# Kernel tuning notes

Measured on AMD Instinct MI355X. Metric: run time of the kernel, lower is better.

The kernel has to match this reference:

```python
import jax, jax.numpy as jnp
import numpy as np


def _safe_div(w, n):
    # tf.math.divide_no_nan: returns 0 where denominator is 0
    n = n[:, None]
    return jnp.where(n > 0, w / jnp.where(n > 0, n, 1.0), 0.0)


def setup_inputs() -> dict:
    key = jax.random.key(0)
    x = jax.random.normal(key, (16, 32768, 256), dtype=jnp.float32)
    return {"x": x}


def reference(x):
    # x: [n_models, n_samples, dim]
    n_models = x.shape[0]
    xt = jnp.transpose(x, (1, 0, 2))  # [ns, nm, dim]
    v0 = xt[:, 0, :]
    basis_list = [_safe_div(v0, jnp.linalg.norm(v0, axis=1))]  # each [ns, dim]
    for i in range(1, n_models):
        B = jnp.stack(basis_list, axis=1)              # [ns, i, dim]
        v = xt[:, i, :]                                # [ns, dim]
        coef = jnp.einsum('nd,nid->ni', v, B)          # projections onto basis
        w = v - jnp.einsum('ni,nid->nd', coef, B)      # classical Gram-Schmidt step
        basis_list.append(_safe_div(w, jnp.linalg.norm(w, axis=1)))
    return jnp.stack(basis_list, axis=0)               # [n_models, ns, dim]
```

## Files before the change

### kernel.cpp

```cpp
#include <hip/hip_runtime.h>
#include <hip/hip_bf16.h>


constexpr int NM   = 16;
constexpr int NR   = 32768;
constexpr int D    = 256;
constexpr int D4   = 64;
constexpr int LROW = 264;
constexpr int GROW = 20;

typedef __attribute__((ext_vector_type(8))) short short8v;
typedef __attribute__((ext_vector_type(4))) float f32x4;

__device__ __forceinline__ float rl(float x, int lane) {
    return __builtin_bit_cast(float,
        __builtin_amdgcn_readlane(__builtin_bit_cast(int, x), lane));
}

__device__ __forceinline__ unsigned short bfbits(__hip_bfloat16 h) {
    return __builtin_bit_cast(unsigned short, h);
}

__global__ __launch_bounds__(64) void gs_kernel(const float* __restrict__ x,
                                                float* __restrict__ out) {
    __shared__ __align__(16) unsigned short sm_hi[NM * LROW];
    __shared__ __align__(16) unsigned short sm_lo[NM * LROW];
    __shared__ __align__(16) float          sm_G[NM * GROW];

    const int lane = threadIdx.x;
    const int row  = blockIdx.x;
    const int vec  = lane & 15;
    const int kgrp = lane >> 4;

    const float4* __restrict__ xi = reinterpret_cast<const float4*>(x);
    float4* __restrict__ oo       = reinterpret_cast<float4*>(out);

    float4 v[NM];
#pragma unroll
    for (int i = 0; i < NM; ++i)
        v[i] = xi[(size_t)(i * NR + row) * D4 + lane];

#pragma unroll
    for (int i = 0; i < NM; ++i) {
        float4 f = v[i];
        __hip_bfloat16 h0 = __float2bfloat16(f.x);
        __hip_bfloat16 h1 = __float2bfloat16(f.y);
        __hip_bfloat16 h2 = __float2bfloat16(f.z);
        __hip_bfloat16 h3 = __float2bfloat16(f.w);
        __hip_bfloat16 l0 = __float2bfloat16(f.x - __bfloat162float(h0));
        __hip_bfloat16 l1 = __float2bfloat16(f.y - __bfloat162float(h1));
        __hip_bfloat16 l2 = __float2bfloat16(f.z - __bfloat162float(h2));
        __hip_bfloat16 l3 = __float2bfloat16(f.w - __bfloat162float(h3));
        ushort4 hp = make_ushort4(bfbits(h0), bfbits(h1), bfbits(h2), bfbits(h3));
        ushort4 lp = make_ushort4(bfbits(l0), bfbits(l1), bfbits(l2), bfbits(l3));
        *reinterpret_cast<ushort4*>(&sm_hi[i * LROW + 4 * lane]) = hp;
        *reinterpret_cast<ushort4*>(&sm_lo[i * LROW + 4 * lane]) = lp;
    }
    __syncthreads();

    f32x4 g = {0.0f, 0.0f, 0.0f, 0.0f};
#pragma unroll
    for (int c = 0; c < 8; ++c) {
        const int off = vec * LROW + c * 32 + kgrp * 8;
        short8v ah = *reinterpret_cast<const short8v*>(&sm_hi[off]);
        short8v al = *reinterpret_cast<const short8v*>(&sm_lo[off]);
        g = __builtin_amdgcn_mfma_f32_16x16x32_bf16(ah, ah, g, 0, 0, 0);
        g = __builtin_amdgcn_mfma_f32_16x16x32_bf16(ah, al, g, 0, 0, 0);
        g = __builtin_amdgcn_mfma_f32_16x16x32_bf16(al, ah, g, 0, 0, 0);
    }

#pragma unroll
    for (int r = 0; r < 4; ++r)
        sm_G[(kgrp * 4 + r) * GROW + vec] = g[r];
    __syncthreads();

    float a[NM];
#pragma unroll
    for (int t = 0; t < 4; ++t) {
        f32x4 rr = *reinterpret_cast<const f32x4*>(&sm_G[vec * GROW + t * 4]);
        a[4 * t + 0] = rr[0];
        a[4 * t + 1] = rr[1];
        a[4 * t + 2] = rr[2];
        a[4 * t + 3] = rr[3];
    }

#pragma unroll
    for (int j = 0; j < NM; ++j) {
        float p   = rl(a[j], j);
        float inv = (p > 0.0f) ? rsqrtf(p) : 0.0f;
        v[j].x *= inv; v[j].y *= inv; v[j].z *= inv; v[j].w *= inv;
        oo[(size_t)(j * NR + row) * D4 + lane] = v[j];
        a[j] *= inv;
#pragma unroll
        for (int t = j + 1; t < NM; ++t) {
            float u = rl(a[j], t);
            a[t]  = fmaf(-u, a[j], a[t]);
            v[t].x = fmaf(-u, v[j].x, v[t].x);
            v[t].y = fmaf(-u, v[j].y, v[t].y);
            v[t].z = fmaf(-u, v[j].z, v[t].z);
            v[t].w = fmaf(-u, v[j].w, v[t].w);
        }
    }
}

extern "C" void kernel_launch(void* const* d_in, const int* in_sizes, int n_in,
                              void* d_out, int out_size, void* d_ws, size_t ws_size,
                              hipStream_t stream) {
    const float* x = (const float*)d_in[0];
    float* out     = (float*)d_out;
    dim3 grid(NR);
    dim3 block(64);
    hipLaunchKernelGGL(gs_kernel, grid, block, 0, stream, x, out);
}
```

Baseline: 198.6 us.

## Feed Gram MFMA operands straight from global loads and drop LDS staging

Each lane now loads its MFMA operand fragments directly from global memory (L2/L1 re-reads of the same row already loaded into registers) and splits them into bf16 hi/lo in registers, removing the shared-memory staging and both barriers. The Gram matrix result is redistributed with cross-lane shuffles instead of an LDS round trip, and launch bounds request 4 waves per SIMD. This trades LDS traffic and synchronisation for a second global (cache-hit) read of the input and more register pressure.

```diff
diff --git a/kernel.cpp b/kernel.cpp
--- a/kernel.cpp
+++ b/kernel.cpp
@@ -2,12 +2,9 @@
 #include <hip/hip_bf16.h>
 
 
-constexpr int NM   = 16;
-constexpr int NR   = 32768;
-constexpr int D    = 256;
-constexpr int D4   = 64;
-constexpr int LROW = 264;
-constexpr int GROW = 20;
+constexpr int NM = 16;
+constexpr int NR = 32768;
+constexpr int D4 = 64;
 
 typedef __attribute__((ext_vector_type(8))) short short8v;
 typedef __attribute__((ext_vector_type(4))) float f32x4;
@@ -17,16 +14,12 @@
         __builtin_amdgcn_readlane(__builtin_bit_cast(int, x), lane));
 }
 
-__device__ __forceinline__ unsigned short bfbits(__hip_bfloat16 h) {
-    return __builtin_bit_cast(unsigned short, h);
+__device__ __forceinline__ short bfbits(float f) {
+    return __builtin_bit_cast(short, __float2bfloat16(f));
 }
 
-__global__ __launch_bounds__(64) void gs_kernel(const float* __restrict__ x,
-                                                float* __restrict__ out) {
-    __shared__ __align__(16) unsigned short sm_hi[NM * LROW];
-    __shared__ __align__(16) unsigned short sm_lo[NM * LROW];
-    __shared__ __align__(16) float          sm_G[NM * GROW];
-
+__global__ __launch_bounds__(64, 4) void gs_kernel(const float* __restrict__ x,
+                                                   float* __restrict__ out) {
     const int lane = threadIdx.x;
     const int row  = blockIdx.x;
     const int vec  = lane & 15;
@@ -40,49 +33,30 @@
     for (int i = 0; i < NM; ++i)
         v[i] = xi[(size_t)(i * NR + row) * D4 + lane];
 
-#pragma unroll
-    for (int i = 0; i < NM; ++i) {
-        float4 f = v[i];
-        __hip_bfloat16 h0 = __float2bfloat16(f.x);
-        __hip_bfloat16 h1 = __float2bfloat16(f.y);
-        __hip_bfloat16 h2 = __float2bfloat16(f.z);
-        __hip_bfloat16 h3 = __float2bfloat16(f.w);
-        __hip_bfloat16 l0 = __float2bfloat16(f.x - __bfloat162float(h0));
-        __hip_bfloat16 l1 = __float2bfloat16(f.y - __bfloat162float(h1));
-        __hip_bfloat16 l2 = __float2bfloat16(f.z - __bfloat162float(h2));
-        __hip_bfloat16 l3 = __float2bfloat16(f.w - __bfloat162float(h3));
-        ushort4 hp = make_ushort4(bfbits(h0), bfbits(h1), bfbits(h2), bfbits(h3));
-        ushort4 lp = make_ushort4(bfbits(l0), bfbits(l1), bfbits(l2), bfbits(l3));
-        *reinterpret_cast<ushort4*>(&sm_hi[i * LROW + 4 * lane]) = hp;
-        *reinterpret_cast<ushort4*>(&sm_lo[i * LROW + 4 * lane]) = lp;
-    }
-    __syncthreads();
-
+    const float4* __restrict__ fbase = xi + (size_t)(vec * NR + row) * D4;
     f32x4 g = {0.0f, 0.0f, 0.0f, 0.0f};
 #pragma unroll
     for (int c = 0; c < 8; ++c) {
-        const int off = vec * LROW + c * 32 + kgrp * 8;
-        short8v ah = *reinterpret_cast<const short8v*>(&sm_hi[off]);
-        short8v al = *reinterpret_cast<const short8v*>(&sm_lo[off]);
+        float4 f0 = fbase[c * 8 + kgrp * 2];
+        float4 f1 = fbase[c * 8 + kgrp * 2 + 1];
+        float f[8] = {f0.x, f0.y, f0.z, f0.w, f1.x, f1.y, f1.z, f1.w};
+        short8v ah, al;
+#pragma unroll
+        for (int j = 0; j < 8; ++j) {
+            short hb = bfbits(f[j]);
+            ah[j] = hb;
+            float hv = __bfloat162float(__builtin_bit_cast(__hip_bfloat16, hb));
+            al[j] = bfbits(f[j] - hv);
+        }
         g = __builtin_amdgcn_mfma_f32_16x16x32_bf16(ah, ah, g, 0, 0, 0);
         g = __builtin_amdgcn_mfma_f32_16x16x32_bf16(ah, al, g, 0, 0, 0);
         g = __builtin_amdgcn_mfma_f32_16x16x32_bf16(al, ah, g, 0, 0, 0);
     }
 
-#pragma unroll
-    for (int r = 0; r < 4; ++r)
-        sm_G[(kgrp * 4 + r) * GROW + vec] = g[r];
-    __syncthreads();
-
     float a[NM];
 #pragma unroll
-    for (int t = 0; t < 4; ++t) {
-        f32x4 rr = *reinterpret_cast<const f32x4*>(&sm_G[vec * GROW + t * 4]);
-        a[4 * t + 0] = rr[0];
-        a[4 * t + 1] = rr[1];
-        a[4 * t + 2] = rr[2];
-        a[4 * t + 3] = rr[3];
-    }
+    for (int n = 0; n < NM; ++n)
+        a[n] = __shfl(g[n & 3], vec + 16 * (n >> 2), 64);
 
 #pragma unroll
     for (int j = 0; j < NM; ++j) {
```

New measurement: 247.7 us. +24.7%, slower.
